# Optimization experiments

Measured on AMD Instinct MI355X. Metric: run time of the kernel, lower is better.

Reference implementation:

```python
import jax, jax.numpy as jnp
import numpy as np

HIDDEN = 1024
EMB = HIDDEN // 2          # embedding_dim = hidden_dim // 2
NUM_OPS = 8
BATCH = 16384


def setup_inputs() -> dict:
    key = jax.random.key(0)
    ks = jax.random.split(key, 8)
    x = jax.random.normal(ks[0], (BATCH, HIDDEN), dtype=jnp.float32)
    sampled_ops = jax.random.randint(ks[1], (BATCH,), 0, NUM_OPS, dtype=jnp.int32)
    op_emb = jax.random.normal(ks[2], (NUM_OPS, EMB), dtype=jnp.float32) * 0.02
    # per-expert 2-layer MLP params (Linear stored as [in, out] for x @ W)
    s1 = 1.0 / np.sqrt(HIDDEN + EMB)
    s2 = 1.0 / np.sqrt(HIDDEN)
    W1 = jax.random.uniform(ks[3], (NUM_OPS, HIDDEN + EMB, HIDDEN), jnp.float32, -s1, s1)
    b1 = jax.random.uniform(ks[4], (NUM_OPS, HIDDEN), jnp.float32, -s1, s1)
    W2 = jax.random.uniform(ks[5], (NUM_OPS, HIDDEN, HIDDEN), jnp.float32, -s2, s2)
    b2 = jax.random.uniform(ks[6], (NUM_OPS, HIDDEN), jnp.float32, -s2, s2)
    return {"x": x, "sampled_ops": sampled_ops, "op_emb": op_emb,
            "W1": W1, "b1": b1, "W2": W2, "b2": b2}


def reference(x, sampled_ops, op_emb, W1, b1, W2, b2):
    # gather per-token operator embedding and augment input
    emb = jnp.take(op_emb, sampled_ops, axis=0)            # [B, EMB]
    x_aug = jnp.concatenate([x, emb], axis=-1)             # [B, H+EMB]
    num_ops = W1.shape[0]
    out = jnp.zeros_like(x)
    # loop over the small fixed expert set; mask-combine per token
    for o in range(num_ops):
        h = jax.nn.relu(x_aug @ W1[o] + b1[o])             # [B, H]
        y = jax.nn.relu(h @ W2[o] + b2[o])                 # [B, H]
        mask = (sampled_ops == o)[:, None]
        out = out + jnp.where(mask, y, 0.0)
    return out
```

## Files before the change

kernel.cpp:

```cpp
#include <hip/hip_runtime.h>
#include <hip/hip_bf16.h>

#define BATCH 16384
#define HID   1024
#define EMBD  512
#define NOPS  8
#define MAXT  136
#define CNTS  16

typedef __attribute__((ext_vector_type(8))) short bf16x8;
typedef __attribute__((ext_vector_type(4))) float f32x4;

__device__ __forceinline__ unsigned short f2bf(float f) {
  unsigned int u = __float_as_uint(f);
  u += 0x7FFF + ((u >> 16) & 1);
  return (unsigned short)(u >> 16);
}

__device__ __forceinline__ unsigned int pk2(float a, float b) {
  __hip_bfloat162 t = __float22bfloat162_rn(make_float2(a, b));
  return *(unsigned int*)(&t);
}

__device__ __forceinline__ void lds_load16(void* lds, const void* g) {
  __builtin_amdgcn_global_load_lds(
      (const __attribute__((address_space(1))) unsigned int*)g,
      (__attribute__((address_space(3))) unsigned int*)lds, 16, 0, 0);
}

__device__ __forceinline__ void decode_bid(int bid, int& g, int& nx) {
  g = 17 * (bid & 7) + (bid >> 6);
  nx = (bid >> 3) & 7;
}

__device__ __forceinline__ void w_prep_tile(const float* __restrict__ W,
                                            short* __restrict__ Wp,
                                            int ks, int nx, int tid) {
  int n = tid & 127, kh = tid >> 7;
  const float* src = W + (size_t)(ks * 32 + kh * 16) * 1024 + nx * 128 + n;
  float v[16];
#pragma unroll
  for (int kk = 0; kk < 16; ++kk) v[kk] = src[(size_t)kk * 1024];
  uint4 a, b;
  a.x = pk2(v[0], v[1]);  a.y = pk2(v[2], v[3]);
  a.z = pk2(v[4], v[5]);  a.w = pk2(v[6], v[7]);
  b.x = pk2(v[8], v[9]);  b.y = pk2(v[10], v[11]);
  b.z = pk2(v[12], v[13]); b.w = pk2(v[14], v[15]);
  uint4* dst = (uint4*)Wp;
  dst[(2 * kh) * 128 + n]     = a;
  dst[(2 * kh + 1) * 128 + n] = b;
}

__global__ void bucket_ce_k(const int* __restrict__ ops, int* __restrict__ cnt,
                            int* __restrict__ idx, const float* __restrict__ W1,
                            const float* __restrict__ emb,
                            const float* __restrict__ b1, float* __restrict__ ce,
                            short* __restrict__ W1p) {
  int bid = blockIdx.x;
  int tid = threadIdx.x;
  if (bid >= 192) {
    int b = bid - 192;
    int e = b / 256; int rr = b % 256; int nx = rr / 32, ks = rr % 32;
    w_prep_tile(W1 + (size_t)e * 1536 * 1024,
                W1p + ((size_t)(e * 8 + nx) * 32 + ks) * 4096, ks, nx, tid);
    return;
  }
  if (bid >= 64) {
    int cb = bid - 64;
    int e = cb >> 4, kp = cb & 15;
    int n = tid * 4;
    const float* Wc = W1 + (size_t)e * 1536 * 1024 + (size_t)(1024 + kp * 32) * 1024 + n;
    const float* ee = emb + e * EMBD + kp * 32;
    float4 a = make_float4(0.f, 0.f, 0.f, 0.f);
#pragma unroll
    for (int kk = 0; kk < 32; ++kk) {
      float s = ee[kk];
      float4 r = *(const float4*)(Wc + (size_t)kk * 1024);
      a.x += s * r.x; a.y += s * r.y; a.z += s * r.z; a.w += s * r.w;
    }
    if (kp == 0) {
      float4 b = *(const float4*)(b1 + e * HID + n);
      a.x += b.x; a.y += b.y; a.z += b.z; a.w += b.w;
    }
    float* d = ce + e * HID + n;
    atomicAdd(d + 0, a.x); atomicAdd(d + 1, a.y);
    atomicAdd(d + 2, a.z); atomicAdd(d + 3, a.w);
    return;
  }
  __shared__ int wcnt[4][NOPS];
  __shared__ int wbase[4][NOPS];
  int lane = tid & 63, w = tid >> 6;
  int t = bid * 256 + tid;
  int op = ops[t];
  unsigned long long msave = 0;
#pragma unroll
  for (int o = 0; o < NOPS; ++o) {
    unsigned long long mm = __ballot(op == o);
    if (op == o) msave = mm;
    if (lane == o) wcnt[w][o] = __popcll(mm);
  }
  __syncthreads();
  if (tid < NOPS) {
    int c0 = wcnt[0][tid], c1 = wcnt[1][tid], c2 = wcnt[2][tid], c3 = wcnt[3][tid];
    int base = atomicAdd(&cnt[tid * CNTS], c0 + c1 + c2 + c3);
    wbase[0][tid] = base;
    wbase[1][tid] = base + c0;
    wbase[2][tid] = base + c0 + c1;
    wbase[3][tid] = base + c0 + c1 + c2;
  }
  __syncthreads();
  int pre = __popcll(msave & ((1ull << lane) - 1ull));
  idx[op * BATCH + wbase[w][op] + pre] = t;
}

__global__ void schedule_k(const int* __restrict__ cnt, int* __restrict__ desc,
                           int* __restrict__ ntp, int* __restrict__ idx) {
  __shared__ int base[NOPS + 1];
  int tid = threadIdx.x;
  if (tid == 0) {
    int n = 0;
    for (int e = 0; e < NOPS; ++e) { base[e] = n; n += (cnt[e * CNTS] + 127) >> 7; }
    base[NOPS] = n;
    *ntp = n;
  }
  __syncthreads();
  for (int e = 0; e < NOPS; ++e) {
    int b0 = base[e], nt = base[e + 1] - b0;
    for (int t = tid; t < nt; t += 256) {
      desc[2 * (b0 + t)] = e;
      desc[2 * (b0 + t) + 1] = t * 128;
    }
  }
  for (int e = 0; e < NOPS; ++e) {
    int c = cnt[e * CNTS];
    int cp = (c + 127) & ~127;
    for (int p = c + tid; p < cp; p += 256) idx[e * BATCH + p] = 0;
  }
}

__global__ __launch_bounds__(256) void gemm1_w2_k(
    const float* __restrict__ x, const int* __restrict__ idx,
    const float* __restrict__ ce, const short* __restrict__ W1p,
    unsigned short* __restrict__ hp, const int* __restrict__ desc,
    const int* __restrict__ ntp, const float* __restrict__ W2,
    short* __restrict__ W2p) {
  int bid = blockIdx.x;
  int tid = threadIdx.x;
  if (bid >= 8 * MAXT) {
    int b = bid - 8 * MAXT;
    int e = b / 256; int rr = b % 256; int nx = rr / 32, ks = rr % 32;
    w_prep_tile(W2 + (size_t)e * 1024 * 1024,
                W2p + ((size_t)(e * 8 + nx) * 32 + ks) * 4096, ks, nx, tid);
    return;
  }
  int g, nx;
  decode_bid(bid, g, nx);
  if (g >= *ntp) return;
  int e = desc[2 * g], rs = desc[2 * g + 1];

  __shared__ __align__(16) char smem[16384];
  __shared__ int toks[128];
  short* lA = (short*)smem;
  short* lB = (short*)(smem + 8192);

  int lane = tid & 63, w = tid >> 6;
  int wm = w >> 1, wn = w & 1;
  int fr = lane & 15, fq = lane >> 4;
  int ar = tid >> 1, ah = tid & 1;

  if (tid < 128) toks[tid] = idx[e * BATCH + rs + tid];
  __syncthreads();
  const float* xrow = x + (size_t)toks[ar] * HID + ah * 16;
  const char* Bsrc = (const char*)W1p + (size_t)(e * 8 + nx) * 32 * 8192;

  f32x4 acc[4][4] = {};
  float4 fa0 = ((const float4*)xrow)[0];
  float4 fa1 = ((const float4*)xrow)[1];
  float4 fa2 = ((const float4*)xrow)[2];
  float4 fa3 = ((const float4*)xrow)[3];

  for (int ks = 0; ks < 32; ++ks) {
    const char* bs = Bsrc + ks * 8192;
    lds_load16(smem + 8192 + w * 1024, bs + w * 1024 + lane * 16);
    lds_load16(smem + 12288 + w * 1024, bs + 4096 + w * 1024 + lane * 16);
    uint4 p0 = make_uint4(pk2(fa0.x, fa0.y), pk2(fa0.z, fa0.w),
                          pk2(fa1.x, fa1.y), pk2(fa1.z, fa1.w));
    uint4 p1 = make_uint4(pk2(fa2.x, fa2.y), pk2(fa2.z, fa2.w),
                          pk2(fa3.x, fa3.y), pk2(fa3.z, fa3.w));
    *(uint4*)&lA[((2 * ah) * 128 + ar) * 8] = p0;
    *(uint4*)&lA[((2 * ah + 1) * 128 + ar) * 8] = p1;
    __syncthreads();
    if (ks < 31) {
      const float4* src = (const float4*)(xrow + (ks + 1) * 32);
      fa0 = src[0]; fa1 = src[1]; fa2 = src[2]; fa3 = src[3];
    }
    bf16x8 af[4], bfr[4];
#pragma unroll
    for (int i = 0; i < 4; ++i)
      af[i] = *(const bf16x8*)&lA[(fq * 128 + wm * 64 + i * 16 + fr) * 8];
#pragma unroll
    for (int j = 0; j < 4; ++j)
      bfr[j] = *(const bf16x8*)&lB[(fq * 128 + wn * 64 + j * 16 + fr) * 8];
#pragma unroll
    for (int i = 0; i < 4; ++i)
#pragma unroll
      for (int j = 0; j < 4; ++j)
        acc[i][j] = __builtin_amdgcn_mfma_f32_16x16x32_bf16(af[i], bfr[j], acc[i][j], 0, 0, 0);
    __syncthreads();
  }

  float bias[4];
#pragma unroll
  for (int j = 0; j < 4; ++j)
    bias[j] = ce[e * HID + nx * 128 + wn * 64 + j * 16 + fr];

  int lr = lane >> 2;
#pragma unroll
  for (int i = 0; i < 4; ++i) {
    __syncthreads();
#pragma unroll
    for (int j = 0; j < 4; ++j)
#pragma unroll
      for (int rg = 0; rg < 4; ++rg) {
        float v = acc[i][j][rg] + bias[j];
        v = v > 0.f ? v : 0.f;
        int row16 = fq * 4 + rg;
        int off = w * 2048 + row16 * 128 + (j * 16 + fr) * 2;
        off ^= (row16 & 1) << 6;
        *(unsigned short*)(smem + off) = f2bf(v);
      }
    __syncthreads();
    int R = wm * 64 + i * 16 + lr;
#pragma unroll
    for (int s = 0; s < 2; ++s) {
      int ch = (lane & 3) + s * 4;
      int off = w * 2048 + lr * 128 + ch * 16;
      off ^= (lr & 1) << 6;
      uint4 val = *(const uint4*)(smem + off);
      int ks2 = nx * 4 + wn * 2 + (ch >> 2);
      int kq = ch & 3;
      *(uint4*)(hp + (((size_t)(g * 32 + ks2) * 4 + kq) * 128 + R) * 8) = val;
    }
  }
}

__global__ __launch_bounds__(256) void gemm2_k(
    const unsigned short* __restrict__ hp, const float* __restrict__ b2,
    const short* __restrict__ W2p, float* __restrict__ out,
    const int* __restrict__ idx, const int* __restrict__ cnt,
    const int* __restrict__ desc, const int* __restrict__ ntp) {
  int g, nx;
  decode_bid(blockIdx.x, g, nx);
  if (g >= *ntp) return;
  int e = desc[2 * g], rs = desc[2 * g + 1];
  int ce2 = cnt[e * CNTS];

  __shared__ __align__(16) char smem[16384];
  __shared__ int toks[128];
  short* lA = (short*)smem;
  short* lB = (short*)(smem + 8192);

  int tid = threadIdx.x, lane = tid & 63, w = tid >> 6;
  int wm = w >> 1, wn = w & 1;
  int fr = lane & 15, fq = lane >> 4;

  if (tid < 128) toks[tid] = idx[e * BATCH + rs + tid];

  const char* Asrc = (const char*)hp + (size_t)g * 32 * 8192;
  const char* Bsrc = (const char*)W2p + (size_t)(e * 8 + nx) * 32 * 8192;

  f32x4 acc[4][4] = {};

  for (int ks = 0; ks < 32; ++ks) {
    const char* as = Asrc + ks * 8192;
    const char* bs = Bsrc + ks * 8192;
    lds_load16(smem + w * 1024, as + w * 1024 + lane * 16);
    lds_load16(smem + 4096 + w * 1024, as + 4096 + w * 1024 + lane * 16);
    lds_load16(smem + 8192 + w * 1024, bs + w * 1024 + lane * 16);
    lds_load16(smem + 12288 + w * 1024, bs + 4096 + w * 1024 + lane * 16);
    __syncthreads();

    bf16x8 af[4], bfr[4];
#pragma unroll
    for (int i = 0; i < 4; ++i)
      af[i] = *(const bf16x8*)&lA[(fq * 128 + wm * 64 + i * 16 + fr) * 8];
#pragma unroll
    for (int j = 0; j < 4; ++j)
      bfr[j] = *(const bf16x8*)&lB[(fq * 128 + wn * 64 + j * 16 + fr) * 8];
#pragma unroll
    for (int i = 0; i < 4; ++i)
#pragma unroll
      for (int j = 0; j < 4; ++j)
        acc[i][j] = __builtin_amdgcn_mfma_f32_16x16x32_bf16(af[i], bfr[j], acc[i][j], 0, 0, 0);
    __syncthreads();
  }

  float bias[4];
#pragma unroll
  for (int j = 0; j < 4; ++j)
    bias[j] = b2[e * HID + nx * 128 + wn * 64 + j * 16 + fr];

  int lr = lane >> 2;
#pragma unroll
  for (int i = 0; i < 4; ++i) {
    __syncthreads();
#pragma unroll
    for (int j = 0; j < 4; ++j)
#pragma unroll
      for (int rg = 0; rg < 4; ++rg) {
        float v = acc[i][j][rg] + bias[j];
        int row16 = fq * 4 + rg;
        int off = w * 4096 + row16 * 256 + (j * 16 + fr) * 4;
        off ^= (row16 & 1) << 6;
        *(float*)(smem + off) = v > 0.f ? v : 0.f;
      }
    __syncthreads();
    int R = wm * 64 + i * 16 + lr;
    if (R < ce2 - rs) {
      float* orow = out + (size_t)toks[R] * HID + nx * 128 + wn * 64;
#pragma unroll
      for (int s = 0; s < 4; ++s) {
        int ch = (lane & 3) + s * 4;
        int off = w * 4096 + lr * 256 + ch * 16;
        off ^= (lr & 1) << 6;
        *(float4*)(orow + ch * 4) = *(const float4*)(smem + off);
      }
    }
  }
}


extern "C" void kernel_launch(void* const* d_in, const int* in_sizes, int n_in,
                              void* d_out, int out_size, void* d_ws, size_t ws_size,
                              hipStream_t stream) {
  const float* x   = (const float*)d_in[0];
  const int*   ops = (const int*)d_in[1];
  const float* emb = (const float*)d_in[2];
  const float* W1  = (const float*)d_in[3];
  const float* b1  = (const float*)d_in[4];
  const float* W2  = (const float*)d_in[5];
  const float* b2  = (const float*)d_in[6];
  float* out = (float*)d_out;

  char* ws = (char*)d_ws;
  int* cnt  = (int*)(ws + 0);
  float* ce = (float*)(ws + 512);
  int* ntp  = (int*)(ws + 33280);
  int* desc = (int*)(ws + 33344);
  int* idx  = (int*)(ws + 36864);
  short* W1p = (short*)(ws + 561152);
  short* W2p = (short*)(ws + 17338368);
  unsigned short* hp = (unsigned short*)(ws + 34115584);

  hipMemsetAsync(ws, 0, 33280, stream);
  bucket_ce_k<<<192 + 2048, 256, 0, stream>>>(ops, cnt, idx, W1, emb, b1, ce, W1p);
  schedule_k<<<1, 256, 0, stream>>>(cnt, desc, ntp, idx);
  gemm1_w2_k<<<8 * MAXT + 2048, 256, 0, stream>>>(x, idx, ce, W1p, hp, desc, ntp, W2, W2p);
  gemm2_k<<<8 * MAXT, 256, 0, stream>>>(hp, b2, W2p, out, idx, cnt, desc, ntp);
}
```

Baseline: 324.4 us.

## Pre-convert x to bf16 and stream gathered A tiles directly into LDS

Adds 4096 blocks to the first kernel that convert all of x from fp32 to bf16 into a workspace buffer. The first GEMM then gathers token rows from that bf16 buffer with direct global-to-LDS loads, replacing per-iteration fp32 loads, register packing and LDS stores. This halves the A-operand bytes read by each of the 8 column tiles and removes conversion work from the GEMM's inner loop. The cost is an extra full pass that reads x and writes a 32 MB bf16 copy, and the inner loop loses the register prefetch of the next A slice.

```diff
diff --git a/kernel.cpp b/kernel.cpp
--- a/kernel.cpp
+++ b/kernel.cpp
@@ -55,9 +55,23 @@
                             int* __restrict__ idx, const float* __restrict__ W1,
                             const float* __restrict__ emb,
                             const float* __restrict__ b1, float* __restrict__ ce,
-                            short* __restrict__ W1p) {
+                            short* __restrict__ W1p, const float* __restrict__ x,
+                            unsigned int* __restrict__ xb) {
   int bid = blockIdx.x;
   int tid = threadIdx.x;
+  if (bid >= 2240) {
+    size_t i = ((size_t)(bid - 2240) * 256 + tid) * 16;
+    const float4* src = (const float4*)(x + i);
+    float4 f0 = src[0], f1 = src[1], f2v = src[2], f3 = src[3];
+    uint4 p0 = make_uint4(pk2(f0.x, f0.y), pk2(f0.z, f0.w),
+                          pk2(f1.x, f1.y), pk2(f1.z, f1.w));
+    uint4 p1 = make_uint4(pk2(f2v.x, f2v.y), pk2(f2v.z, f2v.w),
+                          pk2(f3.x, f3.y), pk2(f3.z, f3.w));
+    uint4* dst = (uint4*)(xb + i / 2);
+    dst[0] = p0;
+    dst[1] = p1;
+    return;
+  }
   if (bid >= 192) {
     int b = bid - 192;
     int e = b / 256; int rr = b % 256; int nx = rr / 32, ks = rr % 32;
@@ -139,7 +153,7 @@
 }
 
 __global__ __launch_bounds__(256) void gemm1_w2_k(
-    const float* __restrict__ x, const int* __restrict__ idx,
+    const unsigned int* __restrict__ xb, const int* __restrict__ idx,
     const float* __restrict__ ce, const short* __restrict__ W1p,
     unsigned short* __restrict__ hp, const int* __restrict__ desc,
     const int* __restrict__ ntp, const float* __restrict__ W2,
@@ -159,41 +173,29 @@
   int e = desc[2 * g], rs = desc[2 * g + 1];
 
   __shared__ __align__(16) char smem[16384];
-  __shared__ int toks[128];
   short* lA = (short*)smem;
   short* lB = (short*)(smem + 8192);
 
   int lane = tid & 63, w = tid >> 6;
   int wm = w >> 1, wn = w & 1;
   int fr = lane & 15, fq = lane >> 4;
-  int ar = tid >> 1, ah = tid & 1;
-
-  if (tid < 128) toks[tid] = idx[e * BATCH + rs + tid];
-  __syncthreads();
-  const float* xrow = x + (size_t)toks[ar] * HID + ah * 16;
+
+  int t0 = idx[e * BATCH + rs + lane];
+  int t1 = idx[e * BATCH + rs + 64 + lane];
+  const char* a0 = (const char*)xb + (size_t)t0 * 2048 + w * 16;
+  const char* a1 = (const char*)xb + (size_t)t1 * 2048 + w * 16;
   const char* Bsrc = (const char*)W1p + (size_t)(e * 8 + nx) * 32 * 8192;
 
   f32x4 acc[4][4] = {};
-  float4 fa0 = ((const float4*)xrow)[0];
-  float4 fa1 = ((const float4*)xrow)[1];
-  float4 fa2 = ((const float4*)xrow)[2];
-  float4 fa3 = ((const float4*)xrow)[3];
 
   for (int ks = 0; ks < 32; ++ks) {
     const char* bs = Bsrc + ks * 8192;
+    lds_load16(smem + w * 2048,        a0 + ks * 64);
+    lds_load16(smem + w * 2048 + 1024, a1 + ks * 64);
     lds_load16(smem + 8192 + w * 1024, bs + w * 1024 + lane * 16);
     lds_load16(smem + 12288 + w * 1024, bs + 4096 + w * 1024 + lane * 16);
-    uint4 p0 = make_uint4(pk2(fa0.x, fa0.y), pk2(fa0.z, fa0.w),
-                          pk2(fa1.x, fa1.y), pk2(fa1.z, fa1.w));
-    uint4 p1 = make_uint4(pk2(fa2.x, fa2.y), pk2(fa2.z, fa2.w),
-                          pk2(fa3.x, fa3.y), pk2(fa3.z, fa3.w));
-    *(uint4*)&lA[((2 * ah) * 128 + ar) * 8] = p0;
-    *(uint4*)&lA[((2 * ah + 1) * 128 + ar) * 8] = p1;
-    __syncthreads();
-    if (ks < 31) {
-      const float4* src = (const float4*)(xrow + (ks + 1) * 32);
-      fa0 = src[0]; fa1 = src[1]; fa2 = src[2]; fa3 = src[3];
-    }
+    __syncthreads();
+
     bf16x8 af[4], bfr[4];
 #pragma unroll
     for (int i = 0; i < 4; ++i)
@@ -351,10 +353,11 @@
   short* W1p = (short*)(ws + 561152);
   short* W2p = (short*)(ws + 17338368);
   unsigned short* hp = (unsigned short*)(ws + 34115584);
+  unsigned int* xb = (unsigned int*)(ws + 69767168);
 
   hipMemsetAsync(ws, 0, 33280, stream);
-  bucket_ce_k<<<192 + 2048, 256, 0, stream>>>(ops, cnt, idx, W1, emb, b1, ce, W1p);
+  bucket_ce_k<<<2240 + 4096, 256, 0, stream>>>(ops, cnt, idx, W1, emb, b1, ce, W1p, x, xb);
   schedule_k<<<1, 256, 0, stream>>>(cnt, desc, ntp, idx);
-  gemm1_w2_k<<<8 * MAXT + 2048, 256, 0, stream>>>(x, idx, ce, W1p, hp, desc, ntp, W2, W2p);
+  gemm1_w2_k<<<8 * MAXT + 2048, 256, 0, stream>>>(xb, idx, ce, W1p, hp, desc, ntp, W2, W2p);
   gemm2_k<<<8 * MAXT, 256, 0, stream>>>(hp, b2, W2p, out, idx, cnt, desc, ntp);
 }
```

Measured after the change: 301.7 us. 1.08x faster.
